# Performance work log

Measured on AMD Instinct MI355X. Metric: run time of the kernel, lower is better.

## Reference

```python
import jax, jax.numpy as jnp
import numpy as np

B, L, D, H = 4, 2048, 1024, 16
HD = D // H
EPS_LN = 1e-12
EPS_Z = 1e-6


def _rope_tables(seq_len, d_model, base=10000.0):
    k_max = d_model // 2
    theta = 1.0 / (base ** (np.arange(k_max, dtype=np.float32) / k_max))
    ang = np.arange(seq_len, dtype=np.float32)[:, None] * theta[None, :]  # [L, D/2]
    return jnp.asarray(np.cos(ang)), jnp.asarray(np.sin(ang))


def _apply_rope(x, cos, sin):
    # x: [B, L, D]; complex rotation on (even, odd) pairs of last dim
    xr, xi = x[..., 0::2], x[..., 1::2]          # [B, L, D/2]
    or_ = xr * cos - xi * sin
    oi = xr * sin + xi * cos
    return jnp.stack([or_, oi], axis=-1).reshape(x.shape)


def _layernorm(x, g, b):
    mu = jnp.mean(x, axis=-1, keepdims=True)
    var = jnp.mean(jnp.square(x - mu), axis=-1, keepdims=True)
    return (x - mu) * jax.lax.rsqrt(var + EPS_LN) * g + b


def _heads(t):
    # [B, L, D] -> [B, H, L, HD]
    return t.reshape(B, L, H, HD).transpose(0, 2, 1, 3)


def _attn(x, W_qk, b_qk, conv_w, conv_b, cos, sin):
    # x: [B, L, D] (output of in_proj)
    qk = x @ W_qk + b_qk                                  # [B, L, 2D]
    q = jax.nn.elu(qk[..., :D]) + 1.0
    k = jax.nn.elu(qk[..., D:]) + 1.0
    v = x
    q_rope = _heads(_apply_rope(q, cos, sin))             # [B, H, L, HD]
    k_rope = _heads(_apply_rope(k, cos, sin))
    qh, kh, vh = _heads(q), _heads(k), _heads(v)
    # normalizer: 1 / (q . mean_L(k))
    k_mean = jnp.mean(kh, axis=2)                          # [B, H, HD]
    z = 1.0 / (jnp.einsum('bhld,bhd->bhl', qh, k_mean) + EPS_Z)  # [B, H, L]
    # kv accumulation (global, scaled by 1/L via two L^-0.5 factors)
    kv = jnp.einsum('bhld,bhle->bhde', k_rope, vh) / L     # [B, H, HD, HD]
    out = jnp.einsum('bhld,bhde->bhle', q_rope, kv) * z[..., None]  # [B,H,L,HD]
    out = out.transpose(0, 2, 1, 3).reshape(B, L, D)
    # depthwise causal conv + SiLU on v (left pad k-1=3, keep length L)
    v_t = v.transpose(0, 2, 1)                             # [B, D, L]
    conv = jax.lax.conv_general_dilated(
        v_t, conv_w, window_strides=(1,), padding=[(3, 0)],
        dimension_numbers=('NCH', 'OIH', 'NCH'), feature_group_count=D)
    conv = jax.nn.silu(conv + conv_b[:, None])             # [B, D, L]
    return out + conv.transpose(0, 2, 1)


def setup_inputs() -> dict:
    key = jax.random.key(0)
    ks = jax.random.split(key, 12)
    s = 0.02
    return {
        'x': jax.random.normal(ks[0], (B, L, D), jnp.float32),
        'ln1_g': jnp.ones((D,), jnp.float32), 'ln1_b': jnp.zeros((D,), jnp.float32),
        'ln2_g': jnp.ones((D,), jnp.float32), 'ln2_b': jnp.zeros((D,), jnp.float32),
        'W_act': jax.random.normal(ks[1], (D, D), jnp.float32) * s,
        'b_act': jnp.zeros((D,), jnp.float32),
        'W_in': jax.random.normal(ks[2], (D, D), jnp.float32) * s,
        'b_in': jnp.zeros((D,), jnp.float32),
        'W_qk': jax.random.normal(ks[3], (D, 2 * D), jnp.float32) * s,
        'b_qk': jnp.zeros((2 * D,), jnp.float32),
        'conv_w': jax.random.normal(ks[4], (D, 1, 4), jnp.float32) * 0.25,
        'conv_b': jnp.zeros((D,), jnp.float32),
        'W_out': jax.random.normal(ks[5], (D, D), jnp.float32) * s,
        'b_out': jnp.zeros((D,), jnp.float32),
        'W1': jax.random.normal(ks[6], (D, 4 * D), jnp.float32) * s,
        'b1': jnp.zeros((4 * D,), jnp.float32),
        'W2': jax.random.normal(ks[7], (4 * D, D), jnp.float32) * s,
        'b2': jnp.zeros((D,), jnp.float32),
    }


def reference(x, ln1_g, ln1_b, ln2_g, ln2_b, W_act, b_act, W_in, b_in,
              W_qk, b_qk, conv_w, conv_b, W_out, b_out, W1, b1, W2, b2):
    cos, sin = _rope_tables(L, D)
    shortcut = x
    h = _layernorm(x, ln1_g, ln1_b)
    act_res = jax.nn.silu(h @ W_act + b_act)
    h = h @ W_in + b_in
    h = _attn(h, W_qk, b_qk, conv_w, conv_b, cos, sin)
    h = (h * act_res) @ W_out + b_out
    x = shortcut + h
    m = _layernorm(x, ln2_g, ln2_b)
    m = jax.nn.gelu(m @ W1 + b1, approximate=False) @ W2 + b2
    return x + m
```

## Files before the change

### kernel.cpp

```cpp
#include <hip/hip_runtime.h>
#include <math.h>

typedef unsigned short ushort_t;
typedef __attribute__((ext_vector_type(4))) float f32x4;
typedef __attribute__((ext_vector_type(8))) __bf16 bf16x8;
typedef __attribute__((ext_vector_type(8))) unsigned short u16x8;
typedef __attribute__((ext_vector_type(4))) unsigned short u16x4;

#define DEV __device__ __forceinline__

#define CB 4
#define CL 2048
#define CD 1024
#define CH 16
#define CHD 64
#define CM 8192

DEV float bf2f(ushort_t u) {
  unsigned int x = ((unsigned int)u) << 16;
  return __builtin_bit_cast(float, x);
}
DEV ushort_t f2bf(float f) {
  unsigned int u = __builtin_bit_cast(unsigned int, f);
  u += 0x7FFFu + ((u >> 16) & 1u);
  return (ushort_t)(u >> 16);
}
DEV void gload16(const void* g, void* l) {
  __builtin_amdgcn_global_load_lds((const __attribute__((address_space(1))) void*)g,
                                   (__attribute__((address_space(3))) void*)l, 16, 0, 0);
}
DEV bf16x8 frag64(const ushort_t* s, int row, int slog) {
  int sl = slog ^ (row & 7);
  return __builtin_bit_cast(bf16x8, *reinterpret_cast<const u16x8*>(s + row * 64 + sl * 8));
}

__global__ void k_rope_tables(ushort_t* __restrict__ cosT, ushort_t* __restrict__ sinT) {
  int idx = blockIdx.x * 256 + threadIdx.x;
  int l = idx >> 9, j = idx & 511;
  float theta = powf(10000.0f, -(float)j * (1.0f / 512.0f));
  float ang = (float)l * theta;
  float s, c;
  sincosf(ang, &s, &c);
  cosT[idx] = f2bf(c);
  sinT[idx] = f2bf(s);
}

__global__ void k_transpose_bf16(const float* __restrict__ src, ushort_t* __restrict__ dst,
                                 int R, int C) {
  __shared__ float tile[32][33];
  int c0 = blockIdx.x * 32, r0 = blockIdx.y * 32;
  int tx = threadIdx.x & 31, ty = threadIdx.x >> 5;
#pragma unroll
  for (int i = 0; i < 32; i += 8) tile[ty + i][tx] = src[(size_t)(r0 + ty + i) * C + c0 + tx];
  __syncthreads();
#pragma unroll
  for (int i = 0; i < 32; i += 8) dst[(size_t)(c0 + ty + i) * R + r0 + tx] = f2bf(tile[tx][ty + i]);
}

__global__ __launch_bounds__(256) void k_layernorm(const float* __restrict__ x,
                                                   const float* __restrict__ g,
                                                   const float* __restrict__ b,
                                                   ushort_t* __restrict__ out) {
  int row = blockIdx.x, t = threadIdx.x;
  const float* xr = x + (size_t)row * CD;
  f32x4 v = ((const f32x4*)xr)[t];
  float s = v.x + v.y + v.z + v.w;
  float s2 = v.x * v.x + v.y * v.y + v.z * v.z + v.w * v.w;
#pragma unroll
  for (int off = 32; off >= 1; off >>= 1) {
    s += __shfl_xor(s, off);
    s2 += __shfl_xor(s2, off);
  }
  __shared__ float red[8];
  int lane = t & 63, w = t >> 6;
  if (lane == 0) { red[w] = s; red[w + 4] = s2; }
  __syncthreads();
  s = red[0] + red[1] + red[2] + red[3];
  s2 = red[4] + red[5] + red[6] + red[7];
  float mu = s * (1.0f / CD);
  float var = s2 * (1.0f / CD) - mu * mu;
  float rs = rsqrtf(var + 1e-12f);
  f32x4 gg = ((const f32x4*)g)[t];
  f32x4 bb = ((const f32x4*)b)[t];
  u16x4 o;
  o.x = f2bf((v.x - mu) * rs * gg.x + bb.x);
  o.y = f2bf((v.y - mu) * rs * gg.y + bb.y);
  o.z = f2bf((v.z - mu) * rs * gg.z + bb.z);
  o.w = f2bf((v.w - mu) * rs * gg.w + bb.w);
  ((u16x4*)(out + (size_t)row * CD))[t] = o;
}

enum { EP_PLAIN = 0, EP_SILU = 1, EP_ELU1 = 2, EP_GELU = 3, EP_ADDX = 4 };

template <int EP>
__global__ __launch_bounds__(256, 2) void k_gemm(const ushort_t* __restrict__ A,
                                                 const ushort_t* __restrict__ Bt, int N, int K,
                                                 const float* __restrict__ bias,
                                                 const float* __restrict__ addf,
                                                 float* __restrict__ outf,
                                                 ushort_t* __restrict__ outb) {
  __shared__ __align__(16) ushort_t sA[128 * 64];
  __shared__ __align__(16) ushort_t sB[128 * 64];
  const int t = threadIdx.x;
  const int lane = t & 63;
  const int w = t >> 6;
  const int wr = w >> 1, wc = w & 1;
  const int m0 = blockIdx.y * 128, n0 = blockIdx.x * 128;

  f32x4 acc[4][4];
#pragma unroll
  for (int i = 0; i < 4; ++i)
#pragma unroll
    for (int j = 0; j < 4; ++j) acc[i][j] = f32x4{0.f, 0.f, 0.f, 0.f};

  for (int kt = 0; kt < K; kt += 64) {
#pragma unroll
    for (int i = 0; i < 4; ++i) {
      int c = t + i * 256;
      int row = c >> 3;
      int sl = (c & 7) ^ (row & 7);
      int ldsoff = (w * 64 + i * 256) * 8;
      gload16(A + (size_t)(m0 + row) * K + kt + sl * 8, sA + ldsoff);
      gload16(Bt + (size_t)(n0 + row) * K + kt + sl * 8, sB + ldsoff);
    }
    __syncthreads();
#pragma unroll
    for (int kk = 0; kk < 2; ++kk) {
      int slog = kk * 4 + (lane >> 4);
      bf16x8 af[4], bfr[4];
#pragma unroll
      for (int mi = 0; mi < 4; ++mi) af[mi] = frag64(sA, wr * 64 + mi * 16 + (lane & 15), slog);
#pragma unroll
      for (int ni = 0; ni < 4; ++ni) bfr[ni] = frag64(sB, wc * 64 + ni * 16 + (lane & 15), slog);
#pragma unroll
      for (int mi = 0; mi < 4; ++mi)
#pragma unroll
        for (int ni = 0; ni < 4; ++ni)
          acc[mi][ni] =
              __builtin_amdgcn_mfma_f32_16x16x32_bf16(af[mi], bfr[ni], acc[mi][ni], 0, 0, 0);
    }
    __syncthreads();
  }

#pragma unroll
  for (int mi = 0; mi < 4; ++mi) {
#pragma unroll
    for (int ni = 0; ni < 4; ++ni) {
      int col = n0 + wc * 64 + ni * 16 + (lane & 15);
      float bc = bias[col];
#pragma unroll
      for (int r = 0; r < 4; ++r) {
        int row = m0 + wr * 64 + mi * 16 + (lane >> 4) * 4 + r;
        size_t idx = (size_t)row * N + col;
        float vv = acc[mi][ni][r] + bc;
        if constexpr (EP == EP_PLAIN) {
          outb[idx] = f2bf(vv);
        } else if constexpr (EP == EP_SILU) {
          outb[idx] = f2bf(vv / (1.f + expf(-vv)));
        } else if constexpr (EP == EP_ELU1) {
          outb[idx] = f2bf(vv > 0.f ? vv + 1.f : expf(vv));
        } else if constexpr (EP == EP_GELU) {
          outb[idx] = f2bf(0.5f * vv * (1.f + erff(vv * 0.70710678118654752f)));
        } else {
          outf[idx] = addf[idx] + vv;
        }
      }
    }
  }
}

__global__ __launch_bounds__(256) void k_attn_reduce(const ushort_t* __restrict__ qk,
                                                     const ushort_t* __restrict__ vbf,
                                                     const ushort_t* __restrict__ cosT,
                                                     const ushort_t* __restrict__ sinT,
                                                     float* __restrict__ kvpart,
                                                     float* __restrict__ kmpart) {
  int bh = blockIdx.x >> 2, ls = blockIdx.x & 3;
  int b = bh >> 4, h = bh & 15;
  int t = threadIdx.x, lane = t & 63, w = t >> 6;

  __shared__ float kst[64][68];
  __shared__ __align__(16) ushort_t krT[64 * 64];
  __shared__ __align__(16) ushort_t vT[64 * 64];
  __shared__ float cst[64][32];
  __shared__ float snt[64][32];
  __shared__ float kmp[4][64];

  float kmacc = 0.f;
  f32x4 acc[4];
#pragma unroll
  for (int i = 0; i < 4; ++i) acc[i] = f32x4{0.f, 0.f, 0.f, 0.f};

  for (int c = ls * 8; c < ls * 8 + 8; ++c) {
    int l0 = c * 64;
    for (int idx = t; idx < 4096; idx += 256) {
      int l = idx >> 6, d = idx & 63;
      size_t grow = (size_t)(b * CL + l0 + l);
      float kvv = bf2f(qk[grow * 2048 + 1024 + h * 64 + d]);
      kst[l][d] = kvv;
      kmacc += kvv;
      ushort_t vv = vbf[grow * CD + h * 64 + d];
      int sl = (l >> 3) ^ (d & 7);
      vT[d * 64 + sl * 8 + (l & 7)] = vv;
    }
    for (int idx = t; idx < 2048; idx += 256) {
      int l = idx >> 5, j = idx & 31;
      size_t p = (size_t)(l0 + l) * 512 + h * 32 + j;
      cst[l][j] = bf2f(cosT[p]);
      snt[l][j] = bf2f(sinT[p]);
    }
    __syncthreads();
    for (int idx = t; idx < 4096; idx += 256) {
      int l = idx >> 6, d = idx & 63, j = d >> 1;
      float cc = cst[l][j], sn = snt[l][j];
      float kr = (d & 1) ? (kst[l][d - 1] * sn + kst[l][d] * cc)
                         : (kst[l][d] * cc - kst[l][d + 1] * sn);
      int sl = (l >> 3) ^ (d & 7);
      krT[d * 64 + sl * 8 + (l & 7)] = f2bf(kr);
    }
    __syncthreads();
#pragma unroll
    for (int kk = 0; kk < 2; ++kk) {
      int slog = kk * 4 + (lane >> 4);
      bf16x8 a = frag64(vT, w * 16 + (lane & 15), slog);
#pragma unroll
      for (int ni = 0; ni < 4; ++ni) {
        bf16x8 bb = frag64(krT, ni * 16 + (lane & 15), slog);
        acc[ni] = __builtin_amdgcn_mfma_f32_16x16x32_bf16(a, bb, acc[ni], 0, 0, 0);
      }
    }
    __syncthreads();
  }
  float* kp = kvpart + ((size_t)(bh * 4 + ls)) * 4096;
#pragma unroll
  for (int ni = 0; ni < 4; ++ni) {
    int d = ni * 16 + (lane & 15);
#pragma unroll
    for (int r = 0; r < 4; ++r) {
      int e = w * 16 + (lane >> 4) * 4 + r;
      kp[e * 64 + d] = acc[ni][r];
    }
  }
  kmp[t >> 6][t & 63] = kmacc;
  __syncthreads();
  if (t < 64) kmpart[(bh * 4 + ls) * 64 + t] = kmp[0][t] + kmp[1][t] + kmp[2][t] + kmp[3][t];
}

__global__ void k_kv_reduce(const float* __restrict__ kvpart, const float* __restrict__ kmpart,
                            ushort_t* __restrict__ kvT, float* __restrict__ kmean) {
  int gid = blockIdx.x * 256 + threadIdx.x;
  int bh = gid >> 12, r = gid & 4095;
  float s = 0.f;
#pragma unroll
  for (int ls = 0; ls < 4; ++ls) s += kvpart[((size_t)(bh * 4 + ls)) * 4096 + r];
  kvT[gid] = f2bf(s);
  if (gid < 64 * 64) {
    int bh2 = gid >> 6, d = gid & 63;
    float m = 0.f;
#pragma unroll
    for (int ls = 0; ls < 4; ++ls) m += kmpart[(bh2 * 4 + ls) * 64 + d];
    kmean[gid] = m;
  }
}

__global__ __launch_bounds__(256) void k_attn_out(const ushort_t* __restrict__ qk,
                                                  const ushort_t* __restrict__ kvT,
                                                  const float* __restrict__ kmean,
                                                  const ushort_t* __restrict__ cosT,
                                                  const ushort_t* __restrict__ sinT,
                                                  float* __restrict__ outlin) {
  int bid = blockIdx.x;
  int bh = bid >> 5, lt = bid & 31;
  int b = bh >> 4, h = bh & 15;
  int l0 = lt * 64;
  int t = threadIdx.x, lane = t & 63, w = t >> 6;

  __shared__ float qst[64][68];
  __shared__ __align__(16) ushort_t qrT[64 * 64];
  __shared__ __align__(16) ushort_t kvs[64 * 64];
  __shared__ float cst[64][32];
  __shared__ float snt[64][32];
  __shared__ float kms[64];
  __shared__ float zrow[64];

  if (t < 64) kms[t] = kmean[bh * 64 + t];
  for (int idx = t; idx < 4096; idx += 256) {
    int l = idx >> 6, d = idx & 63;
    qst[l][d] = bf2f(qk[(size_t)(b * CL + l0 + l) * 2048 + h * 64 + d]);
    ushort_t kvv = kvT[(size_t)bh * 4096 + idx];
    int e = idx >> 6, dd = idx & 63;
    int sl = (dd >> 3) ^ (e & 7);
    kvs[e * 64 + sl * 8 + (dd & 7)] = kvv;
  }
  for (int idx = t; idx < 2048; idx += 256) {
    int l = idx >> 5, j = idx & 31;
    size_t p = (size_t)(l0 + l) * 512 + h * 32 + j;
    cst[l][j] = bf2f(cosT[p]);
    snt[l][j] = bf2f(sinT[p]);
  }
  __syncthreads();
  for (int idx = t; idx < 4096; idx += 256) {
    int l = idx >> 6, d = idx & 63, j = d >> 1;
    float cc = cst[l][j], sn = snt[l][j];
    float qr = (d & 1) ? (qst[l][d - 1] * sn + qst[l][d] * cc)
                       : (qst[l][d] * cc - qst[l][d + 1] * sn);
    int sl = (d >> 3) ^ (l & 7);
    qrT[l * 64 + sl * 8 + (d & 7)] = f2bf(qr);
  }
  if (t < 64) {
    float dot = 0.f;
#pragma unroll
    for (int d = 0; d < 64; ++d) dot += qst[t][d] * kms[d];
    zrow[t] = 1.0f / (dot * (1.0f / (float)CL) + 1e-6f);
  }
  __syncthreads();
  f32x4 acc[4];
#pragma unroll
  for (int i = 0; i < 4; ++i) acc[i] = f32x4{0.f, 0.f, 0.f, 0.f};
#pragma unroll
  for (int kk = 0; kk < 2; ++kk) {
    int slog = kk * 4 + (lane >> 4);
    bf16x8 a = frag64(qrT, w * 16 + (lane & 15), slog);
#pragma unroll
    for (int ni = 0; ni < 4; ++ni) {
      bf16x8 bb = frag64(kvs, ni * 16 + (lane & 15), slog);
      acc[ni] = __builtin_amdgcn_mfma_f32_16x16x32_bf16(a, bb, acc[ni], 0, 0, 0);
    }
  }
#pragma unroll
  for (int ni = 0; ni < 4; ++ni) {
    int e = ni * 16 + (lane & 15);
#pragma unroll
    for (int r = 0; r < 4; ++r) {
      int l = w * 16 + (lane >> 4) * 4 + r;
      float val = acc[ni][r] * zrow[l] * (1.0f / (float)CL);
      outlin[(size_t)(b * CL + l0 + l) * CD + h * 64 + e] = val;
    }
  }
}

__global__ void k_conv_mul(const float* __restrict__ outlin, const ushort_t* __restrict__ vbf,
                           const ushort_t* __restrict__ act, const float* __restrict__ convw,
                           const float* __restrict__ convb, ushort_t* __restrict__ A4) {
  int idx = blockIdx.x * 256 + threadIdx.x;
  int d = idx & 1023;
  int bl = idx >> 10;
  int l = bl & 2047;
  float accv = 0.f;
#pragma unroll
  for (int tt = 0; tt < 4; ++tt) {
    int ll = l - 3 + tt;
    if (ll >= 0) accv += bf2f(vbf[(size_t)(bl - 3 + tt) * CD + d]) * convw[d * 4 + tt];
  }
  accv += convb[d];
  accv = accv / (1.f + expf(-accv));
  float a4 = (outlin[idx] + accv) * bf2f(act[idx]);
  A4[idx] = f2bf(a4);
}

extern "C" void kernel_launch(void* const* d_in, const int* in_sizes, int n_in, void* d_out,
                              int out_size, void* d_ws, size_t ws_size, hipStream_t stream) {
  const float* x = (const float*)d_in[0];
  const float* ln1_g = (const float*)d_in[1];
  const float* ln1_b = (const float*)d_in[2];
  const float* ln2_g = (const float*)d_in[3];
  const float* ln2_b = (const float*)d_in[4];
  const float* W_act = (const float*)d_in[5];
  const float* b_act = (const float*)d_in[6];
  const float* W_in = (const float*)d_in[7];
  const float* b_in = (const float*)d_in[8];
  const float* W_qk = (const float*)d_in[9];
  const float* b_qk = (const float*)d_in[10];
  const float* conv_w = (const float*)d_in[11];
  const float* conv_b = (const float*)d_in[12];
  const float* W_out = (const float*)d_in[13];
  const float* b_out = (const float*)d_in[14];
  const float* W1 = (const float*)d_in[15];
  const float* b1 = (const float*)d_in[16];
  const float* W2 = (const float*)d_in[17];
  const float* b2 = (const float*)d_in[18];
  float* out = (float*)d_out;

  char* w = (char*)d_ws;
  size_t off = 0;
  auto alloc = [&](size_t bytes) {
    void* p = (void*)(w + off);
    off += (bytes + 255) & ~(size_t)255;
    return p;
  };
  const size_t MB = 1024 * 1024;
  ushort_t* cosT = (ushort_t*)alloc((size_t)CL * 512 * 2);
  ushort_t* sinT = (ushort_t*)alloc((size_t)CL * 512 * 2);
  ushort_t* WactT = (ushort_t*)alloc((size_t)1024 * 1024 * 2);
  ushort_t* WinT = (ushort_t*)alloc((size_t)1024 * 1024 * 2);
  ushort_t* WqkT = (ushort_t*)alloc((size_t)2048 * 1024 * 2);
  ushort_t* WoutT = (ushort_t*)alloc((size_t)1024 * 1024 * 2);
  ushort_t* W1T = (ushort_t*)alloc((size_t)4096 * 1024 * 2);
  ushort_t* W2T = (ushort_t*)alloc((size_t)1024 * 4096 * 2);
  ushort_t* kvTb = (ushort_t*)alloc((size_t)64 * 4096 * 2);
  float* kmean = (float*)alloc((size_t)64 * 64 * 4);
  float* kvpart = (float*)alloc((size_t)256 * 4096 * 4);
  float* kmpart = (float*)alloc((size_t)256 * 64 * 4);
  float* x2 = (float*)alloc((size_t)CM * CD * 4);
  char* R1 = (char*)alloc(64 * MB);
  ushort_t* hln = (ushort_t*)R1;
  ushort_t* qkb = (ushort_t*)(R1 + 16 * MB);
  ushort_t* actb = (ushort_t*)(R1 + 48 * MB);
  ushort_t* Gb = (ushort_t*)R1;
  ushort_t* vb = (ushort_t*)alloc(16 * MB);
  char* R2 = (char*)alloc(48 * MB);
  float* outlin = (float*)R2;
  ushort_t* A4 = (ushort_t*)(R2 + 32 * MB);
  ushort_t* mln = (ushort_t*)R2;

  (void)in_sizes; (void)n_in; (void)out_size; (void)ws_size;

  k_rope_tables<<<4096, 256, 0, stream>>>(cosT, sinT);
  k_transpose_bf16<<<dim3(32, 32), 256, 0, stream>>>(W_act, WactT, 1024, 1024);
  k_transpose_bf16<<<dim3(32, 32), 256, 0, stream>>>(W_in, WinT, 1024, 1024);
  k_transpose_bf16<<<dim3(64, 32), 256, 0, stream>>>(W_qk, WqkT, 1024, 2048);
  k_transpose_bf16<<<dim3(32, 32), 256, 0, stream>>>(W_out, WoutT, 1024, 1024);
  k_transpose_bf16<<<dim3(128, 32), 256, 0, stream>>>(W1, W1T, 1024, 4096);
  k_transpose_bf16<<<dim3(32, 128), 256, 0, stream>>>(W2, W2T, 4096, 1024);

  k_layernorm<<<CM, 256, 0, stream>>>(x, ln1_g, ln1_b, hln);

  k_gemm<EP_SILU><<<dim3(8, 64), 256, 0, stream>>>(hln, WactT, 1024, 1024, b_act, nullptr, nullptr, actb);
  k_gemm<EP_PLAIN><<<dim3(8, 64), 256, 0, stream>>>(hln, WinT, 1024, 1024, b_in, nullptr, nullptr, vb);
  k_gemm<EP_ELU1><<<dim3(16, 64), 256, 0, stream>>>(vb, WqkT, 2048, 1024, b_qk, nullptr, nullptr, qkb);

  k_attn_reduce<<<256, 256, 0, stream>>>(qkb, vb, cosT, sinT, kvpart, kmpart);
  k_kv_reduce<<<1024, 256, 0, stream>>>(kvpart, kmpart, kvTb, kmean);
  k_attn_out<<<2048, 256, 0, stream>>>(qkb, kvTb, kmean, cosT, sinT, outlin);
  k_conv_mul<<<32768, 256, 0, stream>>>(outlin, vb, actb, conv_w, conv_b, A4);

  k_gemm<EP_ADDX><<<dim3(8, 64), 256, 0, stream>>>(A4, WoutT, 1024, 1024, b_out, x, x2, nullptr);
  k_layernorm<<<CM, 256, 0, stream>>>(x2, ln2_g, ln2_b, mln);
  k_gemm<EP_GELU><<<dim3(32, 64), 256, 0, stream>>>(mln, W1T, 4096, 1024, b1, nullptr, nullptr, Gb);
  k_gemm<EP_ADDX><<<dim3(8, 64), 256, 0, stream>>>(Gb, W2T, 1024, 4096, b2, x2, out, nullptr);
}
```

Measured before the change: 493.4 us.

## Replace GEMM with 256x256 double-buffered kernel, split-K, and fuse epilogues

Replaces the 128x128 single-buffered GEMM with a 512-thread 256x256 tile kernel. It double-buffers LDS with staged global-to-LDS loads, uses setprio phases and XCD-aware block remapping. The act and in projections are merged into one GEMM with a split epilogue, and the conv/SiLU/multiply step is fused into the attention output kernel. The two N=1024 GEMMs use split-K into partial buffers, reduced by a new add+layernorm kernel and a final add kernel. This cuts launches, intermediate traffic and tail imbalance, at the cost of extra partial-sum traffic and high register and LDS pressure.

```diff
diff --git a/kernel.cpp b/kernel.cpp
--- a/kernel.cpp
+++ b/kernel.cpp
@@ -12,8 +12,6 @@
 #define CB 4
 #define CL 2048
 #define CD 1024
-#define CH 16
-#define CHD 64
 #define CM 8192
 
 DEV float bf2f(ushort_t u) {
@@ -37,7 +35,7 @@
 __global__ void k_rope_tables(ushort_t* __restrict__ cosT, ushort_t* __restrict__ sinT) {
   int idx = blockIdx.x * 256 + threadIdx.x;
   int l = idx >> 9, j = idx & 511;
-  float theta = powf(10000.0f, -(float)j * (1.0f / 512.0f));
+  float theta = exp2f(-(float)j * (13.2877123795494f / 512.0f));
   float ang = (float)l * theta;
   float s, c;
   sincosf(ang, &s, &c);
@@ -90,79 +88,190 @@
   ((u16x4*)(out + (size_t)row * CD))[t] = o;
 }
 
-enum { EP_PLAIN = 0, EP_SILU = 1, EP_ELU1 = 2, EP_GELU = 3, EP_ADDX = 4 };
+__global__ __launch_bounds__(256) void k_addln(const float* __restrict__ x,
+                                               const float* __restrict__ bo,
+                                               const float* __restrict__ P,
+                                               const float* __restrict__ g,
+                                               const float* __restrict__ b,
+                                               float* __restrict__ x2,
+                                               ushort_t* __restrict__ mln) {
+  int row = blockIdx.x, t = threadIdx.x;
+  size_t base = (size_t)row * CD;
+  f32x4 v = ((const f32x4*)(x + base))[t];
+  v += ((const f32x4*)(P + base))[t];
+  v += ((const f32x4*)(P + (size_t)8388608 + base))[t];
+  v += ((const f32x4*)bo)[t];
+  ((f32x4*)(x2 + base))[t] = v;
+  float s = v.x + v.y + v.z + v.w;
+  float s2 = v.x * v.x + v.y * v.y + v.z * v.z + v.w * v.w;
+#pragma unroll
+  for (int off = 32; off >= 1; off >>= 1) {
+    s += __shfl_xor(s, off);
+    s2 += __shfl_xor(s2, off);
+  }
+  __shared__ float red[8];
+  int lane = t & 63, w = t >> 6;
+  if (lane == 0) { red[w] = s; red[w + 4] = s2; }
+  __syncthreads();
+  s = red[0] + red[1] + red[2] + red[3];
+  s2 = red[4] + red[5] + red[6] + red[7];
+  float mu = s * (1.0f / CD);
+  float var = s2 * (1.0f / CD) - mu * mu;
+  float rs = rsqrtf(var + 1e-12f);
+  f32x4 gg = ((const f32x4*)g)[t];
+  f32x4 bb = ((const f32x4*)b)[t];
+  u16x4 o;
+  o.x = f2bf((v.x - mu) * rs * gg.x + bb.x);
+  o.y = f2bf((v.y - mu) * rs * gg.y + bb.y);
+  o.z = f2bf((v.z - mu) * rs * gg.z + bb.z);
+  o.w = f2bf((v.w - mu) * rs * gg.w + bb.w);
+  ((u16x4*)(mln + base))[t] = o;
+}
+
+__global__ void k_final(const float* __restrict__ x2, const float* __restrict__ b2,
+                        const float* __restrict__ P, float* __restrict__ out) {
+  size_t i = (size_t)blockIdx.x * 256 + threadIdx.x;
+  f32x4 v = ((const f32x4*)x2)[i];
+  v += ((const f32x4*)P)[i];
+  v += ((const f32x4*)(P + 8388608))[i];
+  v += ((const f32x4*)b2)[(int)(i & 255)];
+  ((f32x4*)out)[i] = v;
+}
+
+enum { EP_AV = 0, EP_ELU1 = 1, EP_GELU = 2, EP_KS = 3 };
+
+#define STGH(h_, kt_, buf_)                                                 \
+  {                                                                         \
+    gload16(src[2 * (h_)] + (kt_), smem + (buf_)*32768 + dstoff[2 * (h_)]); \
+    gload16(src[2 * (h_) + 1] + (kt_),                                      \
+            smem + (buf_)*32768 + dstoff[2 * (h_) + 1]);                    \
+  }
+
+#define PHASE(mh_, nh_, RA_, RB_, BF_)                                          \
+  {                                                                             \
+    if (RA_) {                                                                  \
+      _Pragma("unroll") for (int mi = 0; mi < 4; ++mi)                          \
+          _Pragma("unroll") for (int kk = 0; kk < 2; ++kk)                      \
+              af[mi][kk] = frag64(sA, wr * 128 + (mh_)*64 + mi * 16 + lr, kk * 4 + lq); \
+    }                                                                           \
+    if (RB_) {                                                                  \
+      _Pragma("unroll") for (int ni = 0; ni < 2; ++ni)                          \
+          _Pragma("unroll") for (int kk = 0; kk < 2; ++kk)                      \
+              BF_[ni][kk] = frag64(sB, wc * 64 + (nh_)*32 + ni * 16 + lr, kk * 4 + lq); \
+    }                                                                           \
+    __builtin_amdgcn_s_setprio(1);                                              \
+    _Pragma("unroll") for (int kk = 0; kk < 2; ++kk)                            \
+        _Pragma("unroll") for (int mi = 0; mi < 4; ++mi)                        \
+            _Pragma("unroll") for (int ni = 0; ni < 2; ++ni)                    \
+                acc[(mh_)*4 + mi][(nh_)*2 + ni] =                               \
+                    __builtin_amdgcn_mfma_f32_16x16x32_bf16(                    \
+                        af[mi][kk], BF_[ni][kk], acc[(mh_)*4 + mi][(nh_)*2 + ni], 0, 0, 0); \
+    __builtin_amdgcn_s_setprio(0);                                              \
+    __builtin_amdgcn_s_barrier();                                               \
+  }
 
 template <int EP>
-__global__ __launch_bounds__(256, 2) void k_gemm(const ushort_t* __restrict__ A,
-                                                 const ushort_t* __restrict__ Bt, int N, int K,
-                                                 const float* __restrict__ bias,
-                                                 const float* __restrict__ addf,
-                                                 float* __restrict__ outf,
-                                                 ushort_t* __restrict__ outb) {
-  __shared__ __align__(16) ushort_t sA[128 * 64];
-  __shared__ __align__(16) ushort_t sB[128 * 64];
+__global__ __launch_bounds__(512, 2) void k_gemm8(
+    const ushort_t* __restrict__ A, const ushort_t* __restrict__ Bt, int N, int lda, int ldb,
+    int Klen, int nbx, int nks, const float* __restrict__ bias, const float* __restrict__ bias2,
+    float* __restrict__ outf, ushort_t* __restrict__ outb, ushort_t* __restrict__ out2) {
+  __shared__ __align__(16) ushort_t smem[2 * 32768];
   const int t = threadIdx.x;
-  const int lane = t & 63;
-  const int w = t >> 6;
-  const int wr = w >> 1, wc = w & 1;
-  const int m0 = blockIdx.y * 128, n0 = blockIdx.x * 128;
-
-  f32x4 acc[4][4];
-#pragma unroll
-  for (int i = 0; i < 4; ++i)
+  const int lane = t & 63, w = t >> 6;
+  const int wr = w >> 2, wc = w & 3;
+  const int lr = lane & 15, lq = lane >> 4;
+
+  int bid = blockIdx.x;
+  int qq = gridDim.x >> 3;
+  int wg = (bid & 7) * qq + (bid >> 3);
+  int ks = wg % nks;
+  int rem = wg / nks;
+  int by = rem / nbx, bx = rem - by * nbx;
+  const int m0 = by << 8, n0 = bx << 8;
+  const int koff = ks * Klen;
+
+  const ushort_t* src[8];
+  int dstoff[8];
+#pragma unroll
+  for (int i = 0; i < 4; ++i) {
+    int c = t + i * 512, row = c >> 3, sl = (c & 7) ^ (row & 7);
+    src[i] = A + (size_t)(m0 + row) * lda + koff + sl * 8;
+    dstoff[i] = (w * 64 + i * 512) * 8;
+    src[4 + i] = Bt + (size_t)(n0 + row) * ldb + koff + sl * 8;
+    dstoff[4 + i] = 16384 + (w * 64 + i * 512) * 8;
+  }
+
+  f32x4 acc[8][4];
+#pragma unroll
+  for (int i = 0; i < 8; ++i)
 #pragma unroll
     for (int j = 0; j < 4; ++j) acc[i][j] = f32x4{0.f, 0.f, 0.f, 0.f};
 
-  for (int kt = 0; kt < K; kt += 64) {
-#pragma unroll
-    for (int i = 0; i < 4; ++i) {
-      int c = t + i * 256;
-      int row = c >> 3;
-      int sl = (c & 7) ^ (row & 7);
-      int ldsoff = (w * 64 + i * 256) * 8;
-      gload16(A + (size_t)(m0 + row) * K + kt + sl * 8, sA + ldsoff);
-      gload16(Bt + (size_t)(n0 + row) * K + kt + sl * 8, sB + ldsoff);
-    }
-    __syncthreads();
-#pragma unroll
-    for (int kk = 0; kk < 2; ++kk) {
-      int slog = kk * 4 + (lane >> 4);
-      bf16x8 af[4], bfr[4];
-#pragma unroll
-      for (int mi = 0; mi < 4; ++mi) af[mi] = frag64(sA, wr * 64 + mi * 16 + (lane & 15), slog);
-#pragma unroll
-      for (int ni = 0; ni < 4; ++ni) bfr[ni] = frag64(sB, wc * 64 + ni * 16 + (lane & 15), slog);
-#pragma unroll
-      for (int mi = 0; mi < 4; ++mi)
-#pragma unroll
-        for (int ni = 0; ni < 4; ++ni)
-          acc[mi][ni] =
-              __builtin_amdgcn_mfma_f32_16x16x32_bf16(af[mi], bfr[ni], acc[mi][ni], 0, 0, 0);
-    }
-    __syncthreads();
-  }
-
-#pragma unroll
-  for (int mi = 0; mi < 4; ++mi) {
+  const int NT = Klen >> 6;
+  STGH(0, 0, 0);
+  STGH(1, 0, 0);
+  STGH(2, 0, 0);
+  STGH(3, 0, 0);
+  if (NT > 1) {
+    STGH(0, 64, 1);
+    asm volatile("s_waitcnt vmcnt(2)" ::: "memory");
+  } else {
+    asm volatile("s_waitcnt vmcnt(0)" ::: "memory");
+  }
+  __builtin_amdgcn_s_barrier();
+  __builtin_amdgcn_sched_barrier(0);
+
+  bf16x8 af[4][2], bf0[2][2], bf1[2][2];
+  for (int tt = 0; tt < NT; ++tt) {
+    const int buf = tt & 1, nbuf = buf ^ 1;
+    const int ktn = (tt + 1) << 6;
+    const ushort_t* sA = smem + buf * 32768;
+    const ushort_t* sB = sA + 16384;
+    const bool more = (tt + 1 < NT);
+    if (more) STGH(1, ktn, nbuf);
+    PHASE(0, 0, 1, 1, bf0)
+    if (more) STGH(2, ktn, nbuf);
+    PHASE(0, 1, 0, 1, bf1)
+    if (more) STGH(3, ktn, nbuf);
+    PHASE(1, 1, 1, 0, bf1)
+    PHASE(1, 0, 0, 0, bf0)
+    if (more) {
+      if (tt + 2 < NT) {
+        STGH(0, (tt + 2) << 6, buf);
+        asm volatile("s_waitcnt vmcnt(2)" ::: "memory");
+      } else {
+        asm volatile("s_waitcnt vmcnt(0)" ::: "memory");
+      }
+      __builtin_amdgcn_s_barrier();
+      __builtin_amdgcn_sched_barrier(0);
+    }
+  }
+
+#pragma unroll
+  for (int mi = 0; mi < 8; ++mi) {
 #pragma unroll
     for (int ni = 0; ni < 4; ++ni) {
-      int col = n0 + wc * 64 + ni * 16 + (lane & 15);
-      float bc = bias[col];
+      int col = n0 + wc * 64 + ni * 16 + lr;
 #pragma unroll
       for (int r = 0; r < 4; ++r) {
-        int row = m0 + wr * 64 + mi * 16 + (lane >> 4) * 4 + r;
-        size_t idx = (size_t)row * N + col;
-        float vv = acc[mi][ni][r] + bc;
-        if constexpr (EP == EP_PLAIN) {
-          outb[idx] = f2bf(vv);
-        } else if constexpr (EP == EP_SILU) {
-          outb[idx] = f2bf(vv / (1.f + expf(-vv)));
+        int row = m0 + wr * 128 + mi * 16 + lq * 4 + r;
+        float vv = acc[mi][ni][r];
+        if constexpr (EP == EP_AV) {
+          if (col < 1024) {
+            vv += bias[col];
+            outb[(size_t)row * 1024 + col] = f2bf(vv / (1.f + expf(-vv)));
+          } else {
+            vv += bias2[col - 1024];
+            out2[(size_t)row * 1024 + (col - 1024)] = f2bf(vv);
+          }
         } else if constexpr (EP == EP_ELU1) {
-          outb[idx] = f2bf(vv > 0.f ? vv + 1.f : expf(vv));
+          vv += bias[col];
+          outb[(size_t)row * N + col] = f2bf(vv > 0.f ? vv + 1.f : expf(vv));
         } else if constexpr (EP == EP_GELU) {
-          outb[idx] = f2bf(0.5f * vv * (1.f + erff(vv * 0.70710678118654752f)));
+          vv += bias[col];
+          outb[(size_t)row * N + col] = f2bf(0.5f * vv * (1.f + erff(vv * 0.70710678118654752f)));
         } else {
-          outf[idx] = addf[idx] + vv;
+          outf[(size_t)ks * 8388608 + (size_t)row * 1024 + col] = vv;
         }
       }
     }
@@ -249,7 +358,8 @@
 __global__ void k_kv_reduce(const float* __restrict__ kvpart, const float* __restrict__ kmpart,
                             ushort_t* __restrict__ kvT, float* __restrict__ kmean) {
   int gid = blockIdx.x * 256 + threadIdx.x;
-  int bh = gid >> 12, r = gid & 4095;
+  int bh = gid >> 12;
+  int r = gid & 4095;
   float s = 0.f;
 #pragma unroll
   for (int ls = 0; ls < 4; ++ls) s += kvpart[((size_t)(bh * 4 + ls)) * 4096 + r];
@@ -263,12 +373,12 @@
   }
 }
 
-__global__ __launch_bounds__(256) void k_attn_out(const ushort_t* __restrict__ qk,
-                                                  const ushort_t* __restrict__ kvT,
-                                                  const float* __restrict__ kmean,
-                                                  const ushort_t* __restrict__ cosT,
-                                                  const ushort_t* __restrict__ sinT,
-                                                  float* __restrict__ outlin) {
+__global__ __launch_bounds__(256) void k_attn_out(
+    const ushort_t* __restrict__ qk, const ushort_t* __restrict__ kvT,
+    const float* __restrict__ kmean, const ushort_t* __restrict__ cosT,
+    const ushort_t* __restrict__ sinT, const ushort_t* __restrict__ vbf,
+    const ushort_t* __restrict__ act, const float* __restrict__ convw,
+    const float* __restrict__ convb, ushort_t* __restrict__ A4) {
   int bid = blockIdx.x;
   int bh = bid >> 5, lt = bid & 31;
   int b = bh >> 4, h = bh & 15;
@@ -330,32 +440,23 @@
 #pragma unroll
   for (int ni = 0; ni < 4; ++ni) {
     int e = ni * 16 + (lane & 15);
+    int dcol = h * 64 + e;
 #pragma unroll
     for (int r = 0; r < 4; ++r) {
       int l = w * 16 + (lane >> 4) * 4 + r;
+      int lg = l0 + l;
+      size_t row = (size_t)(b * CL + lg);
       float val = acc[ni][r] * zrow[l] * (1.0f / (float)CL);
-      outlin[(size_t)(b * CL + l0 + l) * CD + h * 64 + e] = val;
-    }
-  }
-}
-
-__global__ void k_conv_mul(const float* __restrict__ outlin, const ushort_t* __restrict__ vbf,
-                           const ushort_t* __restrict__ act, const float* __restrict__ convw,
-                           const float* __restrict__ convb, ushort_t* __restrict__ A4) {
-  int idx = blockIdx.x * 256 + threadIdx.x;
-  int d = idx & 1023;
-  int bl = idx >> 10;
-  int l = bl & 2047;
-  float accv = 0.f;
-#pragma unroll
-  for (int tt = 0; tt < 4; ++tt) {
-    int ll = l - 3 + tt;
-    if (ll >= 0) accv += bf2f(vbf[(size_t)(bl - 3 + tt) * CD + d]) * convw[d * 4 + tt];
-  }
-  accv += convb[d];
-  accv = accv / (1.f + expf(-accv));
-  float a4 = (outlin[idx] + accv) * bf2f(act[idx]);
-  A4[idx] = f2bf(a4);
+      float cv = convb[dcol];
+#pragma unroll
+      for (int tt = 0; tt < 4; ++tt) {
+        if (lg - 3 + tt >= 0) cv += bf2f(vbf[(row - 3 + tt) * CD + dcol]) * convw[dcol * 4 + tt];
+      }
+      cv = cv / (1.f + expf(-cv));
+      float a4 = (val + cv) * bf2f(act[row * CD + dcol]);
+      A4[row * CD + dcol] = f2bf(a4);
+    }
+  }
 }
 
 extern "C" void kernel_launch(void* const* d_in, const int* in_sizes, int n_in, void* d_out,
@@ -382,42 +483,33 @@
   float* out = (float*)d_out;
 
   char* w = (char*)d_ws;
-  size_t off = 0;
-  auto alloc = [&](size_t bytes) {
-    void* p = (void*)(w + off);
-    off += (bytes + 255) & ~(size_t)255;
-    return p;
-  };
   const size_t MB = 1024 * 1024;
-  ushort_t* cosT = (ushort_t*)alloc((size_t)CL * 512 * 2);
-  ushort_t* sinT = (ushort_t*)alloc((size_t)CL * 512 * 2);
-  ushort_t* WactT = (ushort_t*)alloc((size_t)1024 * 1024 * 2);
-  ushort_t* WinT = (ushort_t*)alloc((size_t)1024 * 1024 * 2);
-  ushort_t* WqkT = (ushort_t*)alloc((size_t)2048 * 1024 * 2);
-  ushort_t* WoutT = (ushort_t*)alloc((size_t)1024 * 1024 * 2);
-  ushort_t* W1T = (ushort_t*)alloc((size_t)4096 * 1024 * 2);
-  ushort_t* W2T = (ushort_t*)alloc((size_t)1024 * 4096 * 2);
-  ushort_t* kvTb = (ushort_t*)alloc((size_t)64 * 4096 * 2);
-  float* kmean = (float*)alloc((size_t)64 * 64 * 4);
-  float* kvpart = (float*)alloc((size_t)256 * 4096 * 4);
-  float* kmpart = (float*)alloc((size_t)256 * 64 * 4);
-  float* x2 = (float*)alloc((size_t)CM * CD * 4);
-  char* R1 = (char*)alloc(64 * MB);
-  ushort_t* hln = (ushort_t*)R1;
-  ushort_t* qkb = (ushort_t*)(R1 + 16 * MB);
-  ushort_t* actb = (ushort_t*)(R1 + 48 * MB);
-  ushort_t* Gb = (ushort_t*)R1;
-  ushort_t* vb = (ushort_t*)alloc(16 * MB);
-  char* R2 = (char*)alloc(48 * MB);
-  float* outlin = (float*)R2;
-  ushort_t* A4 = (ushort_t*)(R2 + 32 * MB);
-  ushort_t* mln = (ushort_t*)R2;
+  ushort_t* cosT = (ushort_t*)(w + 0 * MB);
+  ushort_t* sinT = (ushort_t*)(w + 2 * MB);
+  ushort_t* WabT = (ushort_t*)(w + 4 * MB);
+  ushort_t* WqkT = (ushort_t*)(w + 8 * MB);
+  ushort_t* WoutT = (ushort_t*)(w + 12 * MB);
+  ushort_t* kvTb = (ushort_t*)(w + 14 * MB);
+  float* kmean = (float*)(w + 14 * MB + 512 * 1024);
+  float* kmpart = (float*)(w + 14 * MB + 640 * 1024);
+  ushort_t* mln = (ushort_t*)(w + 0 * MB);
+  ushort_t* W1T = (ushort_t*)(w + 16 * MB);
+  ushort_t* W2T = (ushort_t*)(w + 24 * MB);
+  ushort_t* hln = (ushort_t*)(w + 32 * MB);
+  ushort_t* qkb = (ushort_t*)(w + 48 * MB);
+  ushort_t* actb = (ushort_t*)(w + 80 * MB);
+  ushort_t* Gb = (ushort_t*)(w + 32 * MB);
+  ushort_t* vb = (ushort_t*)(w + 96 * MB);
+  ushort_t* A4 = (ushort_t*)(w + 112 * MB);
+  float* kvpart = (float*)(w + 112 * MB);
+  float* x2 = (float*)(w + 96 * MB);
+  float* PP = (float*)(w + 128 * MB);
 
   (void)in_sizes; (void)n_in; (void)out_size; (void)ws_size;
 
   k_rope_tables<<<4096, 256, 0, stream>>>(cosT, sinT);
-  k_transpose_bf16<<<dim3(32, 32), 256, 0, stream>>>(W_act, WactT, 1024, 1024);
-  k_transpose_bf16<<<dim3(32, 32), 256, 0, stream>>>(W_in, WinT, 1024, 1024);
+  k_transpose_bf16<<<dim3(32, 32), 256, 0, stream>>>(W_act, WabT, 1024, 1024);
+  k_transpose_bf16<<<dim3(32, 32), 256, 0, stream>>>(W_in, WabT + (size_t)1024 * 1024, 1024, 1024);
   k_transpose_bf16<<<dim3(64, 32), 256, 0, stream>>>(W_qk, WqkT, 1024, 2048);
   k_transpose_bf16<<<dim3(32, 32), 256, 0, stream>>>(W_out, WoutT, 1024, 1024);
   k_transpose_bf16<<<dim3(128, 32), 256, 0, stream>>>(W1, W1T, 1024, 4096);
@@ -425,17 +517,21 @@
 
   k_layernorm<<<CM, 256, 0, stream>>>(x, ln1_g, ln1_b, hln);
 
-  k_gemm<EP_SILU><<<dim3(8, 64), 256, 0, stream>>>(hln, WactT, 1024, 1024, b_act, nullptr, nullptr, actb);
-  k_gemm<EP_PLAIN><<<dim3(8, 64), 256, 0, stream>>>(hln, WinT, 1024, 1024, b_in, nullptr, nullptr, vb);
-  k_gemm<EP_ELU1><<<dim3(16, 64), 256, 0, stream>>>(vb, WqkT, 2048, 1024, b_qk, nullptr, nullptr, qkb);
+  k_gemm8<EP_AV><<<dim3(256), 512, 0, stream>>>(hln, WabT, 2048, 1024, 1024, 1024, 8, 1, b_act,
+                                                b_in, nullptr, actb, vb);
+  k_gemm8<EP_ELU1><<<dim3(256), 512, 0, stream>>>(vb, WqkT, 2048, 1024, 1024, 1024, 8, 1, b_qk,
+                                                  nullptr, nullptr, qkb, nullptr);
 
   k_attn_reduce<<<256, 256, 0, stream>>>(qkb, vb, cosT, sinT, kvpart, kmpart);
   k_kv_reduce<<<1024, 256, 0, stream>>>(kvpart, kmpart, kvTb, kmean);
-  k_attn_out<<<2048, 256, 0, stream>>>(qkb, kvTb, kmean, cosT, sinT, outlin);
-  k_conv_mul<<<32768, 256, 0, stream>>>(outlin, vb, actb, conv_w, conv_b, A4);
-
-  k_gemm<EP_ADDX><<<dim3(8, 64), 256, 0, stream>>>(A4, WoutT, 1024, 1024, b_out, x, x2, nullptr);
-  k_layernorm<<<CM, 256, 0, stream>>>(x2, ln2_g, ln2_b, mln);
-  k_gemm<EP_GELU><<<dim3(32, 64), 256, 0, stream>>>(mln, W1T, 4096, 1024, b1, nullptr, nullptr, Gb);
-  k_gemm<EP_ADDX><<<dim3(8, 64), 256, 0, stream>>>(Gb, W2T, 1024, 4096, b2, x2, out, nullptr);
-}
+  k_attn_out<<<2048, 256, 0, stream>>>(qkb, kvTb, kmean, cosT, sinT, vb, actb, conv_w, conv_b, A4);
+
+  k_gemm8<EP_KS><<<dim3(256), 512, 0, stream>>>(A4, WoutT, 1024, 1024, 1024, 512, 4, 2, nullptr,
+                                                nullptr, PP, nullptr, nullptr);
+  k_addln<<<CM, 256, 0, stream>>>(x, b_out, PP, ln2_g, ln2_b, x2, mln);
+  k_gemm8<EP_GELU><<<dim3(512), 512, 0, stream>>>(mln, W1T, 4096, 1024, 1024, 1024, 16, 1, b1,
+                                                  nullptr, nullptr, Gb, nullptr);
+  k_gemm8<EP_KS><<<dim3(256), 512, 0, stream>>>(Gb, W2T, 1024, 4096, 4096, 2048, 4, 2, nullptr,
+                                                nullptr, PP, nullptr, nullptr);
+  k_final<<<8192, 256, 0, stream>>>(x2, b2, PP, out);
+}
```

Measured after the change: 642.7 us. 30.3% more time.

## Fuse prep kernels, merge act/in GEMMs, fold conv into attn output

Applied to the files above, without the earlier changes.

Merges the rope-table and six weight-transpose launches into one k_prep kernel. Concatenates W_act and W_in so that one GEMM produces both the SiLU gate and v. Folds the depthwise conv, SiLU and gating multiply into the attention output kernel, which removes the fp32 outlin round trip and one launch. It also raises the GEMM launch-bounds occupancy hint from 2 to 4 blocks per CU, which may force register spills, and replaces the workspace allocator with fixed offsets that alias buffers.

```diff
diff --git a/kernel.cpp b/kernel.cpp
--- a/kernel.cpp
+++ b/kernel.cpp
@@ -12,8 +12,6 @@
 #define CB 4
 #define CL 2048
 #define CD 1024
-#define CH 16
-#define CHD 64
 #define CM 8192
 
 DEV float bf2f(ushort_t u) {
@@ -34,27 +32,60 @@
   return __builtin_bit_cast(bf16x8, *reinterpret_cast<const u16x8*>(s + row * 64 + sl * 8));
 }
 
-__global__ void k_rope_tables(ushort_t* __restrict__ cosT, ushort_t* __restrict__ sinT) {
-  int idx = blockIdx.x * 256 + threadIdx.x;
-  int l = idx >> 9, j = idx & 511;
-  float theta = powf(10000.0f, -(float)j * (1.0f / 512.0f));
-  float ang = (float)l * theta;
-  float s, c;
-  sincosf(ang, &s, &c);
-  cosT[idx] = f2bf(c);
-  sinT[idx] = f2bf(s);
-}
-
-__global__ void k_transpose_bf16(const float* __restrict__ src, ushort_t* __restrict__ dst,
-                                 int R, int C) {
+DEV void tr_tile(const float* __restrict__ src, ushort_t* __restrict__ dst, int R, int C, int bx,
+                 int by, int t) {
   __shared__ float tile[32][33];
-  int c0 = blockIdx.x * 32, r0 = blockIdx.y * 32;
-  int tx = threadIdx.x & 31, ty = threadIdx.x >> 5;
+  int c0 = bx * 32, r0 = by * 32;
+  int tx = t & 31, ty = t >> 5;
 #pragma unroll
   for (int i = 0; i < 32; i += 8) tile[ty + i][tx] = src[(size_t)(r0 + ty + i) * C + c0 + tx];
   __syncthreads();
 #pragma unroll
   for (int i = 0; i < 32; i += 8) dst[(size_t)(c0 + ty + i) * R + r0 + tx] = f2bf(tile[tx][ty + i]);
+}
+
+__global__ __launch_bounds__(256) void k_prep(const float* __restrict__ W_act,
+                                              const float* __restrict__ W_in,
+                                              const float* __restrict__ W_qk,
+                                              const float* __restrict__ W_out,
+                                              const float* __restrict__ W1,
+                                              const float* __restrict__ W2,
+                                              ushort_t* __restrict__ WabT,
+                                              ushort_t* __restrict__ WqkT,
+                                              ushort_t* __restrict__ WoutT,
+                                              ushort_t* __restrict__ W1T,
+                                              ushort_t* __restrict__ W2T,
+                                              ushort_t* __restrict__ cosT,
+                                              ushort_t* __restrict__ sinT) {
+  int bid = blockIdx.x, t = threadIdx.x;
+  if (bid < 4096) {
+    int idx = bid * 256 + t;
+    int l = idx >> 9, j = idx & 511;
+    float theta = exp2f(-(float)j * (13.2877123795494f / 512.0f));
+    float ang = (float)l * theta;
+    float s, c;
+    sincosf(ang, &s, &c);
+    cosT[idx] = f2bf(c);
+    sinT[idx] = f2bf(s);
+  } else if (bid < 5120) {
+    int lo = bid - 4096;
+    tr_tile(W_act, WabT, 1024, 1024, lo & 31, lo >> 5, t);
+  } else if (bid < 6144) {
+    int lo = bid - 5120;
+    tr_tile(W_in, WabT + (size_t)1024 * 1024, 1024, 1024, lo & 31, lo >> 5, t);
+  } else if (bid < 8192) {
+    int lo = bid - 6144;
+    tr_tile(W_qk, WqkT, 1024, 2048, lo & 63, lo >> 6, t);
+  } else if (bid < 9216) {
+    int lo = bid - 8192;
+    tr_tile(W_out, WoutT, 1024, 1024, lo & 31, lo >> 5, t);
+  } else if (bid < 13312) {
+    int lo = bid - 9216;
+    tr_tile(W1, W1T, 1024, 4096, lo & 127, lo >> 7, t);
+  } else {
+    int lo = bid - 13312;
+    tr_tile(W2, W2T, 4096, 1024, lo & 31, lo >> 5, t);
+  }
 }
 
 __global__ __launch_bounds__(256) void k_layernorm(const float* __restrict__ x,
@@ -90,15 +121,17 @@
   ((u16x4*)(out + (size_t)row * CD))[t] = o;
 }
 
-enum { EP_PLAIN = 0, EP_SILU = 1, EP_ELU1 = 2, EP_GELU = 3, EP_ADDX = 4 };
+enum { EP_AV = 0, EP_ELU1 = 1, EP_GELU = 2, EP_ADDX = 3 };
 
 template <int EP>
-__global__ __launch_bounds__(256, 2) void k_gemm(const ushort_t* __restrict__ A,
+__global__ __launch_bounds__(256, 4) void k_gemm(const ushort_t* __restrict__ A,
                                                  const ushort_t* __restrict__ Bt, int N, int K,
                                                  const float* __restrict__ bias,
+                                                 const float* __restrict__ bias2,
                                                  const float* __restrict__ addf,
                                                  float* __restrict__ outf,
-                                                 ushort_t* __restrict__ outb) {
+                                                 ushort_t* __restrict__ outb,
+                                                 ushort_t* __restrict__ out2) {
   __shared__ __align__(16) ushort_t sA[128 * 64];
   __shared__ __align__(16) ushort_t sB[128 * 64];
   const int t = threadIdx.x;
@@ -147,22 +180,26 @@
 #pragma unroll
     for (int ni = 0; ni < 4; ++ni) {
       int col = n0 + wc * 64 + ni * 16 + (lane & 15);
-      float bc = bias[col];
 #pragma unroll
       for (int r = 0; r < 4; ++r) {
         int row = m0 + wr * 64 + mi * 16 + (lane >> 4) * 4 + r;
-        size_t idx = (size_t)row * N + col;
-        float vv = acc[mi][ni][r] + bc;
-        if constexpr (EP == EP_PLAIN) {
-          outb[idx] = f2bf(vv);
-        } else if constexpr (EP == EP_SILU) {
-          outb[idx] = f2bf(vv / (1.f + expf(-vv)));
+        if constexpr (EP == EP_AV) {
+          if (col < 1024) {
+            float vv = acc[mi][ni][r] + bias[col];
+            outb[(size_t)row * 1024 + col] = f2bf(vv / (1.f + expf(-vv)));
+          } else {
+            float vv = acc[mi][ni][r] + bias2[col - 1024];
+            out2[(size_t)row * 1024 + (col - 1024)] = f2bf(vv);
+          }
         } else if constexpr (EP == EP_ELU1) {
-          outb[idx] = f2bf(vv > 0.f ? vv + 1.f : expf(vv));
+          float vv = acc[mi][ni][r] + bias[col];
+          outb[(size_t)row * N + col] = f2bf(vv > 0.f ? vv + 1.f : expf(vv));
         } else if constexpr (EP == EP_GELU) {
-          outb[idx] = f2bf(0.5f * vv * (1.f + erff(vv * 0.70710678118654752f)));
+          float vv = acc[mi][ni][r] + bias[col];
+          outb[(size_t)row * N + col] = f2bf(0.5f * vv * (1.f + erff(vv * 0.70710678118654752f)));
         } else {
-          outf[idx] = addf[idx] + vv;
+          size_t idx = (size_t)row * N + col;
+          outf[idx] = addf[idx] + acc[mi][ni][r] + bias[col];
         }
       }
     }
@@ -249,7 +286,8 @@
 __global__ void k_kv_reduce(const float* __restrict__ kvpart, const float* __restrict__ kmpart,
                             ushort_t* __restrict__ kvT, float* __restrict__ kmean) {
   int gid = blockIdx.x * 256 + threadIdx.x;
-  int bh = gid >> 12, r = gid & 4095;
+  int bh = gid >> 12;
+  int r = gid & 4095;
   float s = 0.f;
 #pragma unroll
   for (int ls = 0; ls < 4; ++ls) s += kvpart[((size_t)(bh * 4 + ls)) * 4096 + r];
@@ -263,12 +301,12 @@
   }
 }
 
-__global__ __launch_bounds__(256) void k_attn_out(const ushort_t* __restrict__ qk,
-                                                  const ushort_t* __restrict__ kvT,
-                                                  const float* __restrict__ kmean,
-                                                  const ushort_t* __restrict__ cosT,
-                                                  const ushort_t* __restrict__ sinT,
-                                                  float* __restrict__ outlin) {
+__global__ __launch_bounds__(256) void k_attn_out(
+    const ushort_t* __restrict__ qk, const ushort_t* __restrict__ kvT,
+    const float* __restrict__ kmean, const ushort_t* __restrict__ cosT,
+    const ushort_t* __restrict__ sinT, const ushort_t* __restrict__ vbf,
+    const ushort_t* __restrict__ act, const float* __restrict__ convw,
+    const float* __restrict__ convb, ushort_t* __restrict__ A4) {
   int bid = blockIdx.x;
   int bh = bid >> 5, lt = bid & 31;
   int b = bh >> 4, h = bh & 15;
@@ -330,32 +368,23 @@
 #pragma unroll
   for (int ni = 0; ni < 4; ++ni) {
     int e = ni * 16 + (lane & 15);
+    int dcol = h * 64 + e;
 #pragma unroll
     for (int r = 0; r < 4; ++r) {
       int l = w * 16 + (lane >> 4) * 4 + r;
+      int lg = l0 + l;
+      size_t row = (size_t)(b * CL + lg);
       float val = acc[ni][r] * zrow[l] * (1.0f / (float)CL);
-      outlin[(size_t)(b * CL + l0 + l) * CD + h * 64 + e] = val;
-    }
-  }
-}
-
-__global__ void k_conv_mul(const float* __restrict__ outlin, const ushort_t* __restrict__ vbf,
-                           const ushort_t* __restrict__ act, const float* __restrict__ convw,
-                           const float* __restrict__ convb, ushort_t* __restrict__ A4) {
-  int idx = blockIdx.x * 256 + threadIdx.x;
-  int d = idx & 1023;
-  int bl = idx >> 10;
-  int l = bl & 2047;
-  float accv = 0.f;
-#pragma unroll
-  for (int tt = 0; tt < 4; ++tt) {
-    int ll = l - 3 + tt;
-    if (ll >= 0) accv += bf2f(vbf[(size_t)(bl - 3 + tt) * CD + d]) * convw[d * 4 + tt];
-  }
-  accv += convb[d];
-  accv = accv / (1.f + expf(-accv));
-  float a4 = (outlin[idx] + accv) * bf2f(act[idx]);
-  A4[idx] = f2bf(a4);
+      float cv = convb[dcol];
+#pragma unroll
+      for (int tt = 0; tt < 4; ++tt) {
+        if (lg - 3 + tt >= 0) cv += bf2f(vbf[(row - 3 + tt) * CD + dcol]) * convw[dcol * 4 + tt];
+      }
+      cv = cv / (1.f + expf(-cv));
+      float a4 = (val + cv) * bf2f(act[row * CD + dcol]);
+      A4[row * CD + dcol] = f2bf(a4);
+    }
+  }
 }
 
 extern "C" void kernel_launch(void* const* d_in, const int* in_sizes, int n_in, void* d_out,
@@ -382,60 +411,44 @@
   float* out = (float*)d_out;
 
   char* w = (char*)d_ws;
-  size_t off = 0;
-  auto alloc = [&](size_t bytes) {
-    void* p = (void*)(w + off);
-    off += (bytes + 255) & ~(size_t)255;
-    return p;
-  };
   const size_t MB = 1024 * 1024;
-  ushort_t* cosT = (ushort_t*)alloc((size_t)CL * 512 * 2);
-  ushort_t* sinT = (ushort_t*)alloc((size_t)CL * 512 * 2);
-  ushort_t* WactT = (ushort_t*)alloc((size_t)1024 * 1024 * 2);
-  ushort_t* WinT = (ushort_t*)alloc((size_t)1024 * 1024 * 2);
-  ushort_t* WqkT = (ushort_t*)alloc((size_t)2048 * 1024 * 2);
-  ushort_t* WoutT = (ushort_t*)alloc((size_t)1024 * 1024 * 2);
-  ushort_t* W1T = (ushort_t*)alloc((size_t)4096 * 1024 * 2);
-  ushort_t* W2T = (ushort_t*)alloc((size_t)1024 * 4096 * 2);
-  ushort_t* kvTb = (ushort_t*)alloc((size_t)64 * 4096 * 2);
-  float* kmean = (float*)alloc((size_t)64 * 64 * 4);
-  float* kvpart = (float*)alloc((size_t)256 * 4096 * 4);
-  float* kmpart = (float*)alloc((size_t)256 * 64 * 4);
-  float* x2 = (float*)alloc((size_t)CM * CD * 4);
-  char* R1 = (char*)alloc(64 * MB);
-  ushort_t* hln = (ushort_t*)R1;
-  ushort_t* qkb = (ushort_t*)(R1 + 16 * MB);
-  ushort_t* actb = (ushort_t*)(R1 + 48 * MB);
-  ushort_t* Gb = (ushort_t*)R1;
-  ushort_t* vb = (ushort_t*)alloc(16 * MB);
-  char* R2 = (char*)alloc(48 * MB);
-  float* outlin = (float*)R2;
-  ushort_t* A4 = (ushort_t*)(R2 + 32 * MB);
-  ushort_t* mln = (ushort_t*)R2;
+  ushort_t* cosT = (ushort_t*)(w + 0 * MB);
+  ushort_t* sinT = (ushort_t*)(w + 2 * MB);
+  ushort_t* WabT = (ushort_t*)(w + 4 * MB);
+  ushort_t* WqkT = (ushort_t*)(w + 8 * MB);
+  ushort_t* WoutT = (ushort_t*)(w + 12 * MB);
+  ushort_t* kvTb = (ushort_t*)(w + 14 * MB);
+  float* kmean = (float*)(w + 14 * MB + 512 * 1024);
+  float* kmpart = (float*)(w + 14 * MB + 640 * 1024);
+  ushort_t* mln = (ushort_t*)(w + 0 * MB);
+  ushort_t* W1T = (ushort_t*)(w + 16 * MB);
+  ushort_t* W2T = (ushort_t*)(w + 24 * MB);
+  ushort_t* hln = (ushort_t*)(w + 32 * MB);
+  ushort_t* qkb = (ushort_t*)(w + 48 * MB);
+  ushort_t* actb = (ushort_t*)(w + 80 * MB);
+  ushort_t* Gb = (ushort_t*)(w + 32 * MB);
+  ushort_t* vb = (ushort_t*)(w + 96 * MB);
+  ushort_t* A4 = (ushort_t*)(w + 112 * MB);
+  float* kvpart = (float*)(w + 112 * MB);
+  float* x2 = (float*)(w + 128 * MB);
 
   (void)in_sizes; (void)n_in; (void)out_size; (void)ws_size;
 
-  k_rope_tables<<<4096, 256, 0, stream>>>(cosT, sinT);
-  k_transpose_bf16<<<dim3(32, 32), 256, 0, stream>>>(W_act, WactT, 1024, 1024);
-  k_transpose_bf16<<<dim3(32, 32), 256, 0, stream>>>(W_in, WinT, 1024, 1024);
-  k_transpose_bf16<<<dim3(64, 32), 256, 0, stream>>>(W_qk, WqkT, 1024, 2048);
-  k_transpose_bf16<<<dim3(32, 32), 256, 0, stream>>>(W_out, WoutT, 1024, 1024);
-  k_transpose_bf16<<<dim3(128, 32), 256, 0, stream>>>(W1, W1T, 1024, 4096);
-  k_transpose_bf16<<<dim3(32, 128), 256, 0, stream>>>(W2, W2T, 4096, 1024);
-
+  k_prep<<<17408, 256, 0, stream>>>(W_act, W_in, W_qk, W_out, W1, W2, WabT, WqkT, WoutT, W1T, W2T,
+                                    cosT, sinT);
   k_layernorm<<<CM, 256, 0, stream>>>(x, ln1_g, ln1_b, hln);
-
-  k_gemm<EP_SILU><<<dim3(8, 64), 256, 0, stream>>>(hln, WactT, 1024, 1024, b_act, nullptr, nullptr, actb);
-  k_gemm<EP_PLAIN><<<dim3(8, 64), 256, 0, stream>>>(hln, WinT, 1024, 1024, b_in, nullptr, nullptr, vb);
-  k_gemm<EP_ELU1><<<dim3(16, 64), 256, 0, stream>>>(vb, WqkT, 2048, 1024, b_qk, nullptr, nullptr, qkb);
-
+  k_gemm<EP_AV><<<dim3(16, 64), 256, 0, stream>>>(hln, WabT, 2048, 1024, b_act, b_in, nullptr,
+                                                  nullptr, actb, vb);
+  k_gemm<EP_ELU1><<<dim3(16, 64), 256, 0, stream>>>(vb, WqkT, 2048, 1024, b_qk, nullptr, nullptr,
+                                                    nullptr, qkb, nullptr);
   k_attn_reduce<<<256, 256, 0, stream>>>(qkb, vb, cosT, sinT, kvpart, kmpart);
   k_kv_reduce<<<1024, 256, 0, stream>>>(kvpart, kmpart, kvTb, kmean);
-  k_attn_out<<<2048, 256, 0, stream>>>(qkb, kvTb, kmean, cosT, sinT, outlin);
-  k_conv_mul<<<32768, 256, 0, stream>>>(outlin, vb, actb, conv_w, conv_b, A4);
-
-  k_gemm<EP_ADDX><<<dim3(8, 64), 256, 0, stream>>>(A4, WoutT, 1024, 1024, b_out, x, x2, nullptr);
+  k_attn_out<<<2048, 256, 0, stream>>>(qkb, kvTb, kmean, cosT, sinT, vb, actb, conv_w, conv_b, A4);
+  k_gemm<EP_ADDX><<<dim3(8, 64), 256, 0, stream>>>(A4, WoutT, 1024, 1024, b_out, nullptr, x, x2,
+                                                   nullptr, nullptr);
   k_layernorm<<<CM, 256, 0, stream>>>(x2, ln2_g, ln2_b, mln);
-  k_gemm<EP_GELU><<<dim3(32, 64), 256, 0, stream>>>(mln, W1T, 4096, 1024, b1, nullptr, nullptr, Gb);
-  k_gemm<EP_ADDX><<<dim3(8, 64), 256, 0, stream>>>(Gb, W2T, 1024, 4096, b2, x2, out, nullptr);
-}
+  k_gemm<EP_GELU><<<dim3(32, 64), 256, 0, stream>>>(mln, W1T, 4096, 1024, b1, nullptr, nullptr,
+                                                    nullptr, Gb, nullptr);
+  k_gemm<EP_ADDX><<<dim3(8, 64), 256, 0, stream>>>(Gb, W2T, 1024, 4096, b2, nullptr, x2, out,
+                                                   nullptr, nullptr);
+}
```

Result: faster. 470.7 us (-4.6%).
